# Performance work log

Hardware: AMD Instinct MI355X
Metric: run time of the kernel (lower is better)

The kernel has to match this reference:

```python
import jax, jax.numpy as jnp
import numpy as np

B, C, H, W = 4, 128, 56, 56
K = 7
K2 = K * K
RATIO = 16


def _conv1x1(x, w, b=None):
    # x: [B,C,H,W], w: [O,C]
    y = jnp.einsum('oc,bchw->bohw', w, x)
    return y if b is None else y + b[None, :, None, None]


def _dwconv(x, w, dil, pad):
    # depthwise conv, w: [C,1,k,k]
    return jax.lax.conv_general_dilated(
        x, w, window_strides=(1, 1), padding=[(pad, pad), (pad, pad)],
        rhs_dilation=(dil, dil), feature_group_count=x.shape[1],
        dimension_numbers=('NCHW', 'OIHW', 'NCHW'))


def _bn(x, s, b):
    # inference-mode BatchNorm folded to per-channel affine
    return x * s[None, :, None, None] + b[None, :, None, None]


def setup_inputs() -> dict:
    key = jax.random.key(0)
    ks = jax.random.split(key, 16)
    w = 0.05  # weight scale
    inp = {
        'x_up': jax.random.normal(ks[0], (B, C, H, W), jnp.float32),
        'x_skip': jax.random.normal(ks[1], (B, C, H, W), jnp.float32),
        'wq': jax.random.normal(ks[2], (C, C), jnp.float32) * w,
        'bq': jnp.zeros((C,), jnp.float32),
        'wk': jax.random.normal(ks[3], (C, C), jnp.float32) * w,
        'bk': jnp.zeros((C,), jnp.float32),
        'wv': jax.random.normal(ks[4], (C, C), jnp.float32) * w,
        'bv': jnp.zeros((C,), jnp.float32),
        'ww': jax.random.normal(ks[5], (K2, 49), jnp.float32) * w,
        'bw': jnp.zeros((K2,), jnp.float32),
        'lk_w': jax.random.normal(ks[6], (C, 1, K, K), jnp.float32) * 0.1,
        'lk_bn_s': jax.random.uniform(ks[7], (C,), jnp.float32, 0.5, 1.5),
        'lk_bn_b': jnp.zeros((C,), jnp.float32),
        'dw5': jax.random.normal(ks[8], (C, 1, 5, 5), jnp.float32) * 0.1,
        'bn5_s': jax.random.uniform(ks[7], (C,), jnp.float32, 0.5, 1.5),
        'bn5_b': jnp.zeros((C,), jnp.float32),
        'dw3a': jax.random.normal(ks[9], (C, 1, 3, 3), jnp.float32) * 0.1,
        'bn3a_s': jax.random.uniform(ks[9], (C,), jnp.float32, 0.5, 1.5),
        'bn3a_b': jnp.zeros((C,), jnp.float32),
        'dw3b': jax.random.normal(ks[10], (C, 1, 3, 3), jnp.float32) * 0.1,
        'bn3b_s': jax.random.uniform(ks[10], (C,), jnp.float32, 0.5, 1.5),
        'bn3b_b': jnp.zeros((C,), jnp.float32),
        'dw3c': jax.random.normal(ks[11], (C, 1, 3, 3), jnp.float32) * 0.1,
        'bn3c_s': jax.random.uniform(ks[11], (C,), jnp.float32, 0.5, 1.5),
        'bn3c_b': jnp.zeros((C,), jnp.float32),
        'lepe_bn_s': jax.random.uniform(ks[12], (C,), jnp.float32, 0.5, 1.5),
        'lepe_bn_b': jnp.zeros((C,), jnp.float32),
        'gate_w': jax.random.normal(ks[13], (C, C), jnp.float32) * w,
        'gate_bn_s': jax.random.uniform(ks[13], (C,), jnp.float32, 0.5, 1.5),
        'gate_bn_b': jnp.zeros((C,), jnp.float32),
        'fus_w': jax.random.normal(ks[14], (C, C), jnp.float32) * w,
        'fus_b': jnp.zeros((C,), jnp.float32),
        'ca_w1': jax.random.normal(ks[15], (C // RATIO, C), jnp.float32) * w,
        'ca_w2': jax.random.normal(ks[15], (C, C // RATIO), jnp.float32) * w,
        'res_scale': jnp.ones((1,), jnp.float32),
    }
    return inp


def _forward(x_up, x_skip, wq, bq, wk, bk, wv, bv, ww, bw,
             lk_w, lk_bn_s, lk_bn_b, dw5, bn5_s, bn5_b,
             dw3a, bn3a_s, bn3a_b, dw3b, bn3b_s, bn3b_b, dw3c, bn3c_s, bn3c_b,
             lepe_bn_s, lepe_bn_b, gate_w, gate_bn_s, gate_bn_b,
             fus_w, fus_b, ca_w1, ca_w2, res_scale):
    identity = x_skip

    # ---- lepe: DilatedReparamBlock (lk 7x7 dw + 4 dilated dw branches, each BN) + final BN
    out = _bn(_dwconv(x_skip, lk_w, 1, 3), lk_bn_s, lk_bn_b)
    out = out + _bn(_dwconv(x_skip, dw5, 1, 2), bn5_s, bn5_b)    # k=5, d=1
    out = out + _bn(_dwconv(x_skip, dw3a, 1, 1), bn3a_s, bn3a_b)  # k=3, d=1
    out = out + _bn(_dwconv(x_skip, dw3b, 2, 2), bn3b_s, bn3b_b)  # k=3, d=2
    out = out + _bn(_dwconv(x_skip, dw3c, 3, 3), bn3c_s, bn3c_b)  # k=3, d=3
    lepe = _bn(out, lepe_bn_s, lepe_bn_b)

    # ---- gate: 1x1 conv (no bias) -> BN -> SiLU
    gate = jax.nn.silu(_bn(_conv1x1(x_skip, gate_w), gate_bn_s, gate_bn_b))

    # ---- q / k / v
    query = _conv1x1(x_skip, wq, bq)                              # [B,C,H,W]
    # AdaptiveAvgPool2d(7): H,W divisible by 7 -> block mean
    pooled = x_up.reshape(B, C, 7, H // 7, 7, W // 7).mean(axis=(3, 5))  # [B,C,7,7]
    key_t = _conv1x1(pooled, wk, bk).reshape(B, C, 49)            # [B,C,49]
    value = _conv1x1(x_skip, wv, bv)                              # [B,C,H,W]

    # ---- attention over 49 pooled key tokens
    scale = float(C) ** -0.5
    q_r = query.reshape(B, C, H * W).transpose(0, 2, 1)           # [B,HW,C]
    attn = jax.nn.softmax(jnp.einsum('bnc,bcl->bnl', q_r, key_t) * scale, axis=-1)
    attn_r = attn.transpose(0, 2, 1).reshape(B, 49, H, W)         # [B,49,H,W]
    dyn_w = jnp.einsum('ol,blhw->bohw', ww, attn_r) + bw[None, :, None, None]  # [B,K2,H,W]

    # ---- unfold value (k=7, pad=3), torch layout: channel-major, (kh,kw) row-major
    pad = K // 2
    vp = jnp.pad(value, ((0, 0), (0, 0), (pad, pad), (pad, pad)))
    patches = jnp.stack([vp[:, :, i:i + H, j:j + W]
                         for i in range(K) for j in range(K)], axis=2)  # [B,C,K2,H,W]
    mixed = jnp.einsum('bkhw,bckhw->bchw', dyn_w, patches)

    x_fused = _conv1x1(mixed, fus_w, fus_b) + lepe

    # ---- channel attention (shared MLP on avg & max pooled)
    avg = x_fused.mean(axis=(2, 3))                               # [B,C]
    mx = x_fused.max(axis=(2, 3))                                 # [B,C]
    def ca_mlp(v):
        return jnp.einsum('cr,br->bc', ca_w2, jax.nn.relu(jnp.einsum('rc,bc->br', ca_w1, v)))
    ca = jax.nn.sigmoid(ca_mlp(avg) + ca_mlp(mx))[:, :, None, None]
    x_fused = ca * x_fused

    return gate * x_fused + identity * res_scale


def reference(x_up, x_skip, wq, bq, wk, bk, wv, bv, ww, bw,
              lk_w, lk_bn_s, lk_bn_b, dw5, bn5_s, bn5_b,
              dw3a, bn3a_s, bn3a_b, dw3b, bn3b_s, bn3b_b, dw3c, bn3c_s, bn3c_b,
              lepe_bn_s, lepe_bn_b, gate_w, gate_bn_s, gate_bn_b,
              fus_w, fus_b, ca_w1, ca_w2, res_scale):
    return _forward(x_up, x_skip, wq, bq, wk, bk, wv, bv, ww, bw,
                    lk_w, lk_bn_s, lk_bn_b, dw5, bn5_s, bn5_b,
                    dw3a, bn3a_s, bn3a_b, dw3b, bn3b_s, bn3b_b, dw3c, bn3c_s, bn3c_b,
                    lepe_bn_s, lepe_bn_b, gate_w, gate_bn_s, gate_bn_b,
                    fus_w, fus_b, ca_w1, ca_w2, res_scale)
```

## Files before the change

kernel.cpp:

```cpp
#include <hip/hip_runtime.h>

typedef unsigned int u32;

#define HW 3136
#define SCALE 0.08838834764831843f

#define OFF_W7    0
#define OFF_BIAS  6272
#define OFF_POOL  6400
#define OFF_MT    31488
#define OFF_D     56576
#define OFF_AVG   56772
#define OFF_MAXU  57284
#define OFF_WC    58308
#define OFF_BC    74692
#define OFF_WQKT  74820
#define OFF_DQ    91204
#define OFF_VB    91332
#define OFF_S0    91460
#define OFF_FV    91464
#define OFF_DYN   1697096
#define OFF_XF    2311752

struct Params {
  const float *x_up, *x_skip, *wq, *bq, *wk, *bk, *wv, *bv, *ww, *bw;
  const float *lk_w, *lk_s, *lk_b, *dw5, *s5, *b5, *dw3a, *s3a, *b3a,
              *dw3b, *s3b, *b3b, *dw3c, *s3c, *b3c, *lepe_s, *lepe_b;
  const float *gate_w, *gate_s, *gate_b, *fus_w, *fus_b, *ca_w1, *ca_w2, *res;
  float* W;
  float* out;
};

__device__ __forceinline__ u32 fenc(float f){
  union{float f; u32 u;} v; v.f = f;
  return (v.u & 0x80000000u) ? ~v.u : (v.u | 0x80000000u);
}
__device__ __forceinline__ float fdec(u32 u){
  union{float f; u32 uu;} v;
  v.uu = (u & 0x80000000u) ? (u ^ 0x80000000u) : ~u;
  return v.f;
}

__global__ __launch_bounds__(256) void k_prep(Params P){
  __shared__ float pl[3136];
  __shared__ float part[208];
  float* W = P.W;
  const int tid = threadIdx.x, blk = blockIdx.x;
  if (blk < 512){
    const int b = blk >> 7, c = blk & 127;
    const float* src = P.x_up + (size_t)(b*128 + c)*HW;
    for (int idx = tid; idx < 784; idx += 256)
      *(float4*)&pl[idx*4] = *(const float4*)(src + idx*4);
    __syncthreads();
    if (tid < 196){
      const int l = tid >> 2, s = tid & 3;
      const int i = l/7, j = l%7;
      float sm = 0.f;
      #pragma unroll
      for (int r=0;r<2;++r){
        const int base = (8*i + 2*s + r)*56 + 8*j;
        #pragma unroll
        for (int e=0;e<8;++e) sm += pl[base+e];
      }
      part[tid] = sm;
    }
    __syncthreads();
    if (tid < 49){
      const float sm = part[tid*4] + part[tid*4+1] + part[tid*4+2] + part[tid*4+3];
      W[OFF_POOL + (size_t)(b*128+c)*49 + tid] = sm * (1.f/64.f);
    }
  } else if (blk < 576){
    const int o = (blk-512)*2 + (tid >> 7), c = tid & 127;
    float a = 0.f;
    #pragma unroll 8
    for (int m=0;m<128;++m) a += P.fus_w[o*128+m] * P.wv[m*128+c];
    W[OFF_WC + o*128 + c] = a;
  } else if (blk < 640){
    const int c = (blk-576)*2 + (tid >> 7), k = tid & 127;
    float a = 0.f;
    #pragma unroll 8
    for (int o=0;o<128;++o) a += P.wq[o*128+k] * P.wk[o*128+c];
    W[OFF_WQKT + c*128 + k] = a;
  } else if (blk == 640){
    for (int idx = tid; idx < 6272; idx += 256){
      const int c = idx/49, k = idx%49;
      const int dy = k/7 - 3, dx = k%7 - 3;
      float w = P.lk_s[c] * P.lk_w[c*49 + k];
      if (dy>=-2 && dy<=2 && dx>=-2 && dx<=2)
        w += P.s5[c] * P.dw5[c*25 + (dy+2)*5 + (dx+2)];
      if (dy>=-1 && dy<=1 && dx>=-1 && dx<=1)
        w += P.s3a[c] * P.dw3a[c*9 + (dy+1)*3 + (dx+1)];
      if ((dy==-2||dy==0||dy==2) && (dx==-2||dx==0||dx==2))
        w += P.s3b[c] * P.dw3b[c*9 + (dy/2+1)*3 + (dx/2+1)];
      if ((dy==-3||dy==0||dy==3) && (dx==-3||dx==0||dx==3))
        w += P.s3c[c] * P.dw3c[c*9 + (dy/3+1)*3 + (dx/3+1)];
      W[OFF_W7 + idx] = P.lepe_s[c] * w;
    }
    if (tid < 128){
      const float bs = P.lk_b[tid] + P.b5[tid] + P.b3a[tid] + P.b3b[tid] + P.b3c[tid];
      W[OFF_BIAS + tid] = P.lepe_s[tid] * bs + P.lepe_b[tid] + P.fus_b[tid];
    }
    for (int i = tid; i < 512; i += 256){
      W[OFF_AVG + i] = 0.f;
      ((u32*)W + OFF_MAXU)[i] = fenc(-1e30f);
    }
  } else {
    if (tid < 128){
      float bc = 0.f, dq = 0.f, vb = 0.f;
      #pragma unroll 8
      for (int m=0;m<128;++m){
        bc += P.fus_w[tid*128+m] * P.bv[m];
        dq += P.wq[m*128+tid] * P.bk[m];
        vb += P.bq[m] * P.wk[m*128+tid];
      }
      W[OFF_BC + tid] = bc;
      W[OFF_DQ + tid] = dq;
      W[OFF_VB + tid] = vb;
      if (tid == 0){
        float s = 0.f;
        for (int m=0;m<128;++m) s += P.bq[m]*P.bk[m];
        W[OFF_S0] = s;
      }
    }
  }
}

__global__ __launch_bounds__(128) void k_mt(Params P){
  __shared__ float pc[128], red[128];
  float* W = P.W;
  const int b = blockIdx.x / 49, l = blockIdx.x % 49;
  const int t = threadIdx.x;
  pc[t] = W[OFF_POOL + (size_t)(b*128+t)*49 + l];
  __syncthreads();
  float acc = W[OFF_DQ + t];
  #pragma unroll 8
  for (int c=0;c<128;++c) acc += W[OFF_WQKT + c*128 + t] * pc[c];
  W[OFF_MT + (size_t)b*6272 + t*49 + l] = acc * SCALE;
  red[t] = W[OFF_VB + t] * pc[t];
  __syncthreads();
  if (t < 64) red[t] += red[t+64];
  __syncthreads();
  if (t < 32) red[t] += red[t+32];
  __syncthreads();
  if (t < 16) red[t] += red[t+16];
  __syncthreads();
  if (t < 8) red[t] += red[t+8];
  __syncthreads();
  if (t < 4) red[t] += red[t+4];
  __syncthreads();
  if (t == 0)
    W[OFF_D + b*49 + l] = (red[0]+red[1]+red[2]+red[3] + W[OFF_S0]) * SCALE;
}

__global__ __launch_bounds__(256) void k_qvattn(Params P){
  __shared__ float xl[128][20];
  __shared__ float sh[6272];
  __shared__ float wwl[2401];
  __shared__ float attl[16][52];
  __shared__ float dvl[52];
  float* W = P.W;
  const int tid = threadIdx.x;
  const int x = blockIdx.x, xcd = x & 7;
  const int b = xcd >> 1;
  const int p0 = ((xcd & 1) + 2*(x >> 3)) * 16;

  for (int idx = tid; idx < 512; idx += 256){
    const int c = idx >> 2, pq = idx & 3;
    *(float4*)&xl[c][pq*4] =
        *(const float4*)(P.x_skip + (size_t)(b*128+c)*HW + p0 + pq*4);
  }
  for (int idx = tid; idx < 600; idx += 256)
    *(float4*)&wwl[idx*4] = *(const float4*)(P.ww + idx*4);
  if (tid == 0) wwl[2400] = P.ww[2400];
  if (tid < 49) dvl[tid] = W[OFF_D + b*49 + tid];

  const int oq = tid >> 2, pq = tid & 3;
  const int o0 = oq*2, pxa = pq*4;
  const float i0 = W[OFF_BC + o0], i1 = W[OFF_BC + o0 + 1];
  float a0[4], a1[4];
  #pragma unroll
  for (int j=0;j<4;++j){ a0[j]=i0; a1[j]=i1; }
  for (int g=0; g<4; ++g){
    __syncthreads();
    for (int idx = tid; idx < 1024; idx += 256){
      const int o = idx >> 3, kq = idx & 7;
      const float4 v = *(const float4*)(W + OFF_WC + (size_t)o*128 + g*32 + kq*4);
      sh[(kq*4+0)*133+o] = v.x; sh[(kq*4+1)*133+o] = v.y;
      sh[(kq*4+2)*133+o] = v.z; sh[(kq*4+3)*133+o] = v.w;
    }
    __syncthreads();
    #pragma unroll 8
    for (int k=0;k<32;++k){
      const float2 w2 = *(const float2*)&sh[k*133+o0];
      const float4 x4 = *(const float4*)&xl[g*32+k][pxa];
      const float xv[4] = {x4.x,x4.y,x4.z,x4.w};
      #pragma unroll
      for (int j=0;j<4;++j){ a0[j] += w2.x*xv[j]; a1[j] += w2.y*xv[j]; }
    }
  }
  {
    float4 v0 = {a0[0],a0[1],a0[2],a0[3]};
    float4 v1 = {a1[0],a1[1],a1[2],a1[3]};
    *(float4*)(W + OFF_FV + (size_t)(b*128+o0  )*HW + p0 + pxa) = v0;
    *(float4*)(W + OFF_FV + (size_t)(b*128+o0+1)*HW + p0 + pxa) = v1;
  }

  __syncthreads();
  for (int idx = tid; idx < 1568; idx += 256)
    *(float4*)&sh[idx*4] = *(const float4*)(W + OFF_MT + (size_t)b*6272 + idx*4);
  __syncthreads();

  const int px = tid >> 4, sub = tid & 15;
  const int l0 = sub, l1 = sub+16, l2 = sub+32, l3 = sub+48;
  const int l3c = (l3 < 49) ? l3 : 48;
  float lv0 = dvl[l0], lv1 = dvl[l1], lv2 = dvl[l2];
  float lv3 = (l3 < 49) ? dvl[l3] : -1e30f;
  float a3 = 0.f;
  #pragma unroll 4
  for (int c=0;c<128;++c){
    const float xv = xl[c][px];
    lv0 += sh[c*49+l0]*xv;
    lv1 += sh[c*49+l1]*xv;
    lv2 += sh[c*49+l2]*xv;
    a3  += sh[c*49+l3c]*xv;
  }
  if (l3 < 49) lv3 += a3;

  float m = fmaxf(fmaxf(lv0, lv1), fmaxf(lv2, lv3));
  #pragma unroll
  for (int d=1; d<16; d<<=1) m = fmaxf(m, __shfl_xor(m, d, 64));
  const float e0 = __expf(lv0-m), e1 = __expf(lv1-m), e2 = __expf(lv2-m);
  const float e3 = (l3 < 49) ? __expf(lv3-m) : 0.f;
  float s = e0+e1+e2+e3;
  #pragma unroll
  for (int d=1; d<16; d<<=1) s += __shfl_xor(s, d, 64);
  const float inv = 1.f / s;
  attl[px][l0] = e0*inv;
  attl[px][l1] = e1*inv;
  attl[px][l2] = e2*inv;
  if (l3 < 49) attl[px][l3] = e3*inv;
  __syncthreads();

  #pragma unroll
  for (int j=0;j<4;++j){
    const int oo = sub + 16*j;
    if (oo < 49){
      float a = P.bw[oo];
      #pragma unroll 7
      for (int l=0;l<49;++l) a += wwl[oo*49+l] * attl[px][l];
      W[OFF_DYN + (size_t)(b*49+oo)*HW + p0 + px] = a;
    }
  }
}

__global__ __launch_bounds__(256) void k_mix(Params P){
  __shared__ float fvs[2][20][64];
  __shared__ float xss[2][20][64];
  __shared__ float w7s[2][49];
  float* W = P.W;
  const int tid = threadIdx.x;
  const int blk = blockIdx.x, xcd = blk & 7;
  const int b = xcd >> 1;
  const int idx2 = blk >> 3;
  const int cp = idx2 >> 1;
  const int qt = (xcd & 1) + 2*(idx2 & 1);
  const int c0 = cp*2, r0 = qt*14;

  for (int idx = tid; idx < 1280; idx += 256){
    const int a2 = idx / 320;
    const int ch = a2 & 1, arr = a2 >> 1;
    const int rem = idx % 320;
    const int rr = rem >> 4, cq = rem & 15;
    const int gr = r0 - 3 + rr, gc0 = cq*4 - 4;
    float4 v = {0.f,0.f,0.f,0.f};
    if ((unsigned)gr < 56u){
      const float* src = arr ? (P.x_skip + (size_t)(b*128 + c0 + ch)*HW + gr*56)
                             : (W + OFF_FV + (size_t)(b*128 + c0 + ch)*HW + gr*56);
      if (gc0 >= 0 && gc0 + 3 < 56){
        v = *(const float4*)(src + gc0);
      } else {
        float t[4];
        #pragma unroll
        for (int e=0;e<4;++e){
          const int gc = gc0 + e;
          t[e] = ((unsigned)gc < 56u) ? src[gc] : 0.f;
        }
        v.x=t[0]; v.y=t[1]; v.z=t[2]; v.w=t[3];
      }
    }
    if (arr) *(float4*)&xss[ch][rr][cq*4] = v;
    else     *(float4*)&fvs[ch][rr][cq*4] = v;
  }
  if (tid < 98) w7s[tid/49][tid%49] = W[OFF_W7 + (c0 + tid/49)*49 + tid%49];
  __syncthreads();

  const bool act = tid < 196;
  const int row = tid / 14, q = tid % 14;
  const int q4 = q*4;
  const int grow = r0 + row;
  float acc[2][4];
  {
    const float b0 = W[OFF_BIAS + c0], b1 = W[OFF_BIAS + c0 + 1];
    #pragma unroll
    for (int e=0;e<4;++e){ acc[0][e] = b0; acc[1][e] = b1; }
  }
  if (act){
    const float* dynb = W + OFF_DYN + (size_t)b*49*HW + grow*56 + q4;
    #pragma unroll
    for (int i=0;i<7;++i){
      float4 dr[7];
      #pragma unroll
      for (int j=0;j<7;++j)
        dr[j] = *(const float4*)(dynb + (size_t)(i*7+j)*HW);
      #pragma unroll
      for (int ch=0;ch<2;++ch){
        float fw[12], xw[12];
        {
          float4 t;
          t = *(const float4*)&fvs[ch][row+i][q4];    fw[0]=t.x;fw[1]=t.y;fw[2]=t.z;fw[3]=t.w;
          t = *(const float4*)&fvs[ch][row+i][q4+4];  fw[4]=t.x;fw[5]=t.y;fw[6]=t.z;fw[7]=t.w;
          t = *(const float4*)&fvs[ch][row+i][q4+8];  fw[8]=t.x;fw[9]=t.y;fw[10]=t.z;fw[11]=t.w;
          t = *(const float4*)&xss[ch][row+i][q4];    xw[0]=t.x;xw[1]=t.y;xw[2]=t.z;xw[3]=t.w;
          t = *(const float4*)&xss[ch][row+i][q4+4];  xw[4]=t.x;xw[5]=t.y;xw[6]=t.z;xw[7]=t.w;
          t = *(const float4*)&xss[ch][row+i][q4+8];  xw[8]=t.x;xw[9]=t.y;xw[10]=t.z;xw[11]=t.w;
        }
        #pragma unroll
        for (int j=0;j<7;++j){
          const float4 dv = dr[j];
          const float wv = w7s[ch][i*7+j];
          acc[ch][0] += dv.x*fw[j+1] + wv*xw[j+1];
          acc[ch][1] += dv.y*fw[j+2] + wv*xw[j+2];
          acc[ch][2] += dv.z*fw[j+3] + wv*xw[j+3];
          acc[ch][3] += dv.w*fw[j+4] + wv*xw[j+4];
        }
      }
    }
    #pragma unroll
    for (int ch=0;ch<2;++ch){
      float4 v = {acc[ch][0], acc[ch][1], acc[ch][2], acc[ch][3]};
      *(float4*)(W + OFF_XF + (size_t)(b*128 + c0 + ch)*HW + grow*56 + q4) = v;
    }
  }
  #pragma unroll
  for (int ch=0;ch<2;++ch){
    float s = act ? (acc[ch][0]+acc[ch][1]+acc[ch][2]+acc[ch][3]) : 0.f;
    float mm = act ? fmaxf(fmaxf(acc[ch][0],acc[ch][1]),
                           fmaxf(acc[ch][2],acc[ch][3])) : -1e30f;
    #pragma unroll
    for (int d=1; d<64; d<<=1){
      s += __shfl_xor(s, d, 64);
      mm = fmaxf(mm, __shfl_xor(mm, d, 64));
    }
    if ((tid & 63) == 0){
      atomicAdd(W + OFF_AVG + b*128 + c0 + ch, s);
      atomicMax((u32*)W + OFF_MAXU + b*128 + c0 + ch, fenc(mm));
    }
  }
}

__global__ __launch_bounds__(256) void k_final(Params P){
  __shared__ float xl[128][20];
  __shared__ float wl[32][133];
  __shared__ float hl[16], cal[128];
  float* W = P.W;
  const int tid = threadIdx.x;
  const int x = blockIdx.x, xcd = x & 7;
  const int b = xcd >> 1;
  const int p0 = ((xcd & 1) + 2*(x >> 3)) * 16;

  for (int idx = tid; idx < 512; idx += 256){
    const int c = idx >> 2, pq = idx & 3;
    *(float4*)&xl[c][pq*4] =
        *(const float4*)(P.x_skip + (size_t)(b*128+c)*HW + p0 + pq*4);
  }
  if (tid < 16){
    const int r = tid & 7, which = tid >> 3;
    float a = 0.f;
    #pragma unroll 8
    for (int c=0;c<128;++c){
      const float v = which ? fdec(((u32*)W + OFF_MAXU)[b*128+c])
                            : W[OFF_AVG + b*128+c] * (1.f/3136.f);
      a += P.ca_w1[r*128+c] * v;
    }
    hl[tid] = fmaxf(a, 0.f);
  }
  __syncthreads();
  if (tid < 128){
    float a = 0.f;
    #pragma unroll
    for (int r=0;r<8;++r) a += P.ca_w2[tid*8+r] * (hl[r] + hl[8+r]);
    cal[tid] = 1.f/(1.f + __expf(-a));
  }

  const int oq = tid >> 2, pq = tid & 3;
  const int o0 = oq*2, px = pq*4;
  float a0[4] = {0.f,0.f,0.f,0.f}, a1[4] = {0.f,0.f,0.f,0.f};

  for (int g=0; g<4; ++g){
    __syncthreads();
    for (int idx = tid; idx < 1024; idx += 256){
      const int o = idx >> 3, kq = idx & 7;
      const float4 v = *(const float4*)(P.gate_w + (size_t)o*128 + g*32 + kq*4);
      wl[kq*4+0][o] = v.x; wl[kq*4+1][o] = v.y;
      wl[kq*4+2][o] = v.z; wl[kq*4+3][o] = v.w;
    }
    __syncthreads();
    #pragma unroll 8
    for (int k=0;k<32;++k){
      const float2 w2 = *(const float2*)&wl[k][o0];
      const float4 x4 = *(const float4*)&xl[g*32+k][px];
      const float xv[4] = {x4.x,x4.y,x4.z,x4.w};
      #pragma unroll
      for (int j=0;j<4;++j){ a0[j] += w2.x*xv[j]; a1[j] += w2.y*xv[j]; }
    }
  }
  const float s0 = P.gate_s[o0], s1 = P.gate_s[o0+1];
  const float c0 = P.gate_b[o0], c1 = P.gate_b[o0+1];
  const float ca0 = cal[o0], ca1 = cal[o0+1];
  const float res = P.res[0];
  const float4 xf0 = *(const float4*)(W + OFF_XF + (size_t)(b*128+o0  )*HW + p0 + px);
  const float4 xf1 = *(const float4*)(W + OFF_XF + (size_t)(b*128+o0+1)*HW + p0 + px);
  const float4 sk0 = *(const float4*)&xl[o0][px];
  const float4 sk1 = *(const float4*)&xl[o0+1][px];
  float g0[4] = {a0[0],a0[1],a0[2],a0[3]};
  float g1[4] = {a1[0],a1[1],a1[2],a1[3]};
  #pragma unroll
  for (int j=0;j<4;++j){
    float y0 = s0*g0[j] + c0, y1 = s1*g1[j] + c1;
    g0[j] = y0 / (1.f + __expf(-y0));
    g1[j] = y1 / (1.f + __expf(-y1));
  }
  float4 o0v, o1v;
  o0v.x = g0[0]*ca0*xf0.x + sk0.x*res;
  o0v.y = g0[1]*ca0*xf0.y + sk0.y*res;
  o0v.z = g0[2]*ca0*xf0.z + sk0.z*res;
  o0v.w = g0[3]*ca0*xf0.w + sk0.w*res;
  o1v.x = g1[0]*ca1*xf1.x + sk1.x*res;
  o1v.y = g1[1]*ca1*xf1.y + sk1.y*res;
  o1v.z = g1[2]*ca1*xf1.z + sk1.z*res;
  o1v.w = g1[3]*ca1*xf1.w + sk1.w*res;
  *(float4*)(P.out + (size_t)(b*128+o0  )*HW + p0 + px) = o0v;
  *(float4*)(P.out + (size_t)(b*128+o0+1)*HW + p0 + px) = o1v;
}

extern "C" void kernel_launch(void* const* d_in, const int* in_sizes, int n_in,
                              void* d_out, int out_size, void* d_ws, size_t ws_size,
                              hipStream_t stream){
  Params P;
  const float* const* in = (const float* const*)d_in;
  P.x_up = in[0];  P.x_skip = in[1]; P.wq = in[2];  P.bq = in[3];
  P.wk = in[4];    P.bk = in[5];     P.wv = in[6];  P.bv = in[7];
  P.ww = in[8];    P.bw = in[9];
  P.lk_w = in[10]; P.lk_s = in[11];  P.lk_b = in[12];
  P.dw5 = in[13];  P.s5 = in[14];    P.b5 = in[15];
  P.dw3a = in[16]; P.s3a = in[17];   P.b3a = in[18];
  P.dw3b = in[19]; P.s3b = in[20];   P.b3b = in[21];
  P.dw3c = in[22]; P.s3c = in[23];   P.b3c = in[24];
  P.lepe_s = in[25]; P.lepe_b = in[26];
  P.gate_w = in[27]; P.gate_s = in[28]; P.gate_b = in[29];
  P.fus_w = in[30];  P.fus_b = in[31];
  P.ca_w1 = in[32];  P.ca_w2 = in[33]; P.res = in[34];
  P.W = (float*)d_ws;
  P.out = (float*)d_out;

  hipLaunchKernelGGL(k_prep,   dim3(642), dim3(256), 0, stream, P);
  hipLaunchKernelGGL(k_mt,     dim3(196), dim3(128), 0, stream, P);
  hipLaunchKernelGGL(k_qvattn, dim3(784), dim3(256), 0, stream, P);
  hipLaunchKernelGGL(k_mix,    dim3(1024),dim3(256), 0, stream, P);
  hipLaunchKernelGGL(k_final,  dim3(784), dim3(256), 0, stream, P);
}
```

Measured before the change: 280.5 us.

## Read 1x1 weights directly from global and split k_mt channel reduction

The 1x1 conv GEMMs in k_qvattn and k_final no longer stage transposed weight tiles in shared memory. Each thread now reads its two output rows as float4 directly from global/L2, which removes four sync-and-transpose rounds per block. k_qvattn also loads the MT attention matrix into shared memory up front, overlapping it with the other prologue loads. k_mt uses 256 threads, splits the 128-channel dot product into two halves and replaces the tree reduction with a wavefront shuffle; the trade-off is more global weight traffic per block, which relies on L2 hits.

```diff
diff --git a/kernel.cpp b/kernel.cpp
--- a/kernel.cpp
+++ b/kernel.cpp
@@ -125,31 +125,30 @@
   }
 }
 
-__global__ __launch_bounds__(128) void k_mt(Params P){
-  __shared__ float pc[128], red[128];
+__global__ __launch_bounds__(256) void k_mt(Params P){
+  __shared__ float pc[128];
+  __shared__ float part[256];
   float* W = P.W;
   const int b = blockIdx.x / 49, l = blockIdx.x % 49;
-  const int t = threadIdx.x;
-  pc[t] = W[OFF_POOL + (size_t)(b*128+t)*49 + l];
-  __syncthreads();
-  float acc = W[OFF_DQ + t];
+  const int tid = threadIdx.x;
+  if (tid < 128) pc[tid] = W[OFF_POOL + (size_t)(b*128+tid)*49 + l];
+  __syncthreads();
+  const int t = tid & 127, h = tid >> 7;
+  const int c0 = h*64;
+  float acc = h ? 0.f : W[OFF_DQ + t];
   #pragma unroll 8
-  for (int c=0;c<128;++c) acc += W[OFF_WQKT + c*128 + t] * pc[c];
-  W[OFF_MT + (size_t)b*6272 + t*49 + l] = acc * SCALE;
-  red[t] = W[OFF_VB + t] * pc[t];
-  __syncthreads();
-  if (t < 64) red[t] += red[t+64];
-  __syncthreads();
-  if (t < 32) red[t] += red[t+32];
-  __syncthreads();
-  if (t < 16) red[t] += red[t+16];
-  __syncthreads();
-  if (t < 8) red[t] += red[t+8];
-  __syncthreads();
-  if (t < 4) red[t] += red[t+4];
-  __syncthreads();
-  if (t == 0)
-    W[OFF_D + b*49 + l] = (red[0]+red[1]+red[2]+red[3] + W[OFF_S0]) * SCALE;
+  for (int c=0;c<64;++c) acc += W[OFF_WQKT + (size_t)(c0+c)*128 + t] * pc[c0+c];
+  part[tid] = acc;
+  __syncthreads();
+  if (tid < 128)
+    W[OFF_MT + (size_t)b*6272 + tid*49 + l] = (part[tid] + part[tid+128]) * SCALE;
+  else if (tid < 192){
+    const int u = tid - 128;
+    float r = W[OFF_VB + u]*pc[u] + W[OFF_VB + u+64]*pc[u+64];
+    #pragma unroll
+    for (int d=1; d<64; d<<=1) r += __shfl_xor(r, d, 64);
+    if (u == 0) W[OFF_D + b*49 + l] = (r + W[OFF_S0]) * SCALE;
+  }
 }
 
 __global__ __launch_bounds__(256) void k_qvattn(Params P){
@@ -169,33 +168,34 @@
     *(float4*)&xl[c][pq*4] =
         *(const float4*)(P.x_skip + (size_t)(b*128+c)*HW + p0 + pq*4);
   }
+  for (int idx = tid; idx < 1568; idx += 256)
+    *(float4*)&sh[idx*4] = *(const float4*)(W + OFF_MT + (size_t)b*6272 + idx*4);
   for (int idx = tid; idx < 600; idx += 256)
     *(float4*)&wwl[idx*4] = *(const float4*)(P.ww + idx*4);
   if (tid == 0) wwl[2400] = P.ww[2400];
   if (tid < 49) dvl[tid] = W[OFF_D + b*49 + tid];
+  __syncthreads();
 
   const int oq = tid >> 2, pq = tid & 3;
   const int o0 = oq*2, pxa = pq*4;
+  const float4* __restrict__ wr0 = (const float4*)(W + OFF_WC + (size_t)o0*128);
+  const float4* __restrict__ wr1 = (const float4*)(W + OFF_WC + (size_t)(o0+1)*128);
   const float i0 = W[OFF_BC + o0], i1 = W[OFF_BC + o0 + 1];
   float a0[4], a1[4];
   #pragma unroll
   for (int j=0;j<4;++j){ a0[j]=i0; a1[j]=i1; }
-  for (int g=0; g<4; ++g){
-    __syncthreads();
-    for (int idx = tid; idx < 1024; idx += 256){
-      const int o = idx >> 3, kq = idx & 7;
-      const float4 v = *(const float4*)(W + OFF_WC + (size_t)o*128 + g*32 + kq*4);
-      sh[(kq*4+0)*133+o] = v.x; sh[(kq*4+1)*133+o] = v.y;
-      sh[(kq*4+2)*133+o] = v.z; sh[(kq*4+3)*133+o] = v.w;
-    }
-    __syncthreads();
-    #pragma unroll 8
-    for (int k=0;k<32;++k){
-      const float2 w2 = *(const float2*)&sh[k*133+o0];
-      const float4 x4 = *(const float4*)&xl[g*32+k][pxa];
-      const float xv[4] = {x4.x,x4.y,x4.z,x4.w};
-      #pragma unroll
-      for (int j=0;j<4;++j){ a0[j] += w2.x*xv[j]; a1[j] += w2.y*xv[j]; }
+  #pragma unroll 4
+  for (int g=0; g<32; ++g){
+    const float4 wa = wr0[g], wb = wr1[g];
+    const float wav[4] = {wa.x,wa.y,wa.z,wa.w};
+    const float wbv[4] = {wb.x,wb.y,wb.z,wb.w};
+    #pragma unroll
+    for (int t=0; t<4; ++t){
+      const float4 x4 = *(const float4*)&xl[g*4+t][pxa];
+      a0[0] += wav[t]*x4.x; a0[1] += wav[t]*x4.y;
+      a0[2] += wav[t]*x4.z; a0[3] += wav[t]*x4.w;
+      a1[0] += wbv[t]*x4.x; a1[1] += wbv[t]*x4.y;
+      a1[2] += wbv[t]*x4.z; a1[3] += wbv[t]*x4.w;
     }
   }
   {
@@ -204,11 +204,6 @@
     *(float4*)(W + OFF_FV + (size_t)(b*128+o0  )*HW + p0 + pxa) = v0;
     *(float4*)(W + OFF_FV + (size_t)(b*128+o0+1)*HW + p0 + pxa) = v1;
   }
-
-  __syncthreads();
-  for (int idx = tid; idx < 1568; idx += 256)
-    *(float4*)&sh[idx*4] = *(const float4*)(W + OFF_MT + (size_t)b*6272 + idx*4);
-  __syncthreads();
 
   const int px = tid >> 4, sub = tid & 15;
   const int l0 = sub, l1 = sub+16, l2 = sub+32, l3 = sub+48;
@@ -360,7 +355,6 @@
 
 __global__ __launch_bounds__(256) void k_final(Params P){
   __shared__ float xl[128][20];
-  __shared__ float wl[32][133];
   __shared__ float hl[16], cal[128];
   float* W = P.W;
   const int tid = threadIdx.x;
@@ -394,26 +388,24 @@
 
   const int oq = tid >> 2, pq = tid & 3;
   const int o0 = oq*2, px = pq*4;
+  const float4* __restrict__ wr0 = (const float4*)(P.gate_w + (size_t)o0*128);
+  const float4* __restrict__ wr1 = (const float4*)(P.gate_w + (size_t)(o0+1)*128);
   float a0[4] = {0.f,0.f,0.f,0.f}, a1[4] = {0.f,0.f,0.f,0.f};
-
-  for (int g=0; g<4; ++g){
-    __syncthreads();
-    for (int idx = tid; idx < 1024; idx += 256){
-      const int o = idx >> 3, kq = idx & 7;
-      const float4 v = *(const float4*)(P.gate_w + (size_t)o*128 + g*32 + kq*4);
-      wl[kq*4+0][o] = v.x; wl[kq*4+1][o] = v.y;
-      wl[kq*4+2][o] = v.z; wl[kq*4+3][o] = v.w;
-    }
-    __syncthreads();
-    #pragma unroll 8
-    for (int k=0;k<32;++k){
-      const float2 w2 = *(const float2*)&wl[k][o0];
-      const float4 x4 = *(const float4*)&xl[g*32+k][px];
-      const float xv[4] = {x4.x,x4.y,x4.z,x4.w};
-      #pragma unroll
-      for (int j=0;j<4;++j){ a0[j] += w2.x*xv[j]; a1[j] += w2.y*xv[j]; }
-    }
-  }
+  #pragma unroll 4
+  for (int g=0; g<32; ++g){
+    const float4 wa = wr0[g], wb = wr1[g];
+    const float wav[4] = {wa.x,wa.y,wa.z,wa.w};
+    const float wbv[4] = {wb.x,wb.y,wb.z,wb.w};
+    #pragma unroll
+    for (int t=0; t<4; ++t){
+      const float4 x4 = *(const float4*)&xl[g*4+t][px];
+      a0[0] += wav[t]*x4.x; a0[1] += wav[t]*x4.y;
+      a0[2] += wav[t]*x4.z; a0[3] += wav[t]*x4.w;
+      a1[0] += wbv[t]*x4.x; a1[1] += wbv[t]*x4.y;
+      a1[2] += wbv[t]*x4.z; a1[3] += wbv[t]*x4.w;
+    }
+  }
+  __syncthreads();
   const float s0 = P.gate_s[o0], s1 = P.gate_s[o0+1];
   const float c0 = P.gate_b[o0], c1 = P.gate_b[o0+1];
   const float ca0 = cal[o0], ca1 = cal[o0+1];
@@ -464,7 +456,7 @@
   P.out = (float*)d_out;
 
   hipLaunchKernelGGL(k_prep,   dim3(642), dim3(256), 0, stream, P);
-  hipLaunchKernelGGL(k_mt,     dim3(196), dim3(128), 0, stream, P);
+  hipLaunchKernelGGL(k_mt,     dim3(196), dim3(256), 0, stream, P);
   hipLaunchKernelGGL(k_qvattn, dim3(784), dim3(256), 0, stream, P);
   hipLaunchKernelGGL(k_mix,    dim3(1024),dim3(256), 0, stream, P);
   hipLaunchKernelGGL(k_final,  dim3(784), dim3(256), 0, stream, P);
```

After: 266.0 us. -5.2%, faster.
